# Optimization experiments

Measured on AMD Instinct MI355X. Metric: run time of the kernel, lower is better.

## Reference

```python
import jax, jax.numpy as jnp
import numpy as np

N, L, S, C, H = 4, 2048, 4096, 256, 8
D = C // H          # head dim = 32
HID = 4 * C         # mlp hidden = 1024
LN_EPS = 1e-5
LA_EPS = 1e-6


def _layer_norm(x, g, b):
    m = x.mean(-1, keepdims=True)
    v = ((x - m) ** 2).mean(-1, keepdims=True)
    return (x - m) * jax.lax.rsqrt(v + LN_EPS) * g + b


def _linear_attention(q, k, v):
    # q: [N,L,H,D], k/v: [N,S,H,D]  (elu feature map linear attention)
    Q = jax.nn.elu(q) + 1.0
    K = jax.nn.elu(k) + 1.0
    v_len = v.shape[1]
    KV = jnp.einsum('nshd,nshv->nhdv', K, v / v_len)
    Z = 1.0 / (jnp.einsum('nlhd,nhd->nlh', Q, K.sum(axis=1)) + LA_EPS)
    return jnp.einsum('nlhd,nhdv,nlh->nlhv', Q, KV, Z) * v_len


def setup_inputs() -> dict:
    key = jax.random.key(0)
    ks = jax.random.split(key, 32)
    f32 = jnp.float32
    w = lambda k, *s: (jax.random.normal(k, s, dtype=f32) * 0.02)
    inp = {
        'tgt': jax.random.normal(ks[0], (N, L, C), dtype=f32),
        'memory': jax.random.normal(ks[1], (N, S, C), dtype=f32),
        'tgt_pos': jax.random.normal(ks[2], (N, L, C), dtype=f32),
        'pos_embed': w(ks[3], 1, S, C),
        # layer norms
        'ln1_g': jnp.ones((C,), f32), 'ln1_b': jnp.zeros((C,), f32),
        'ln2_g': jnp.ones((C,), f32), 'ln2_b': jnp.zeros((C,), f32),
        'ln3_g': jnp.ones((C,), f32), 'ln3_b': jnp.zeros((C,), f32),
        # self-attn projections (stored (in,out))
        'wq': w(ks[4], C, C), 'bq': jnp.zeros((C,), f32),
        'wk': w(ks[5], C, C), 'bk': jnp.zeros((C,), f32),
        'wv': w(ks[6], C, C), 'bv': jnp.zeros((C,), f32),
        'w_merge': w(ks[7], C, C),
        # cross-attn (CCAttention) projections
        'cwq': w(ks[8], C, C), 'cbq': jnp.zeros((C,), f32),
        'cwk': w(ks[9], C, C), 'cbk': jnp.zeros((C,), f32),
        'cwv': w(ks[10], C, C), 'cbv': jnp.zeros((C,), f32),
        'cwo': w(ks[11], C, C), 'cbo': jnp.zeros((C,), f32),
        # mlp (fc1 -> dwconv3x3 -> gelu -> fc2)
        'mw1': w(ks[12], C, HID), 'mb1': jnp.zeros((HID,), f32),
        'dw_k': w(ks[13], HID, 1, 3, 3), 'dw_b': jnp.zeros((HID,), f32),
        'mw2': w(ks[14], HID, C), 'mb2': jnp.zeros((C,), f32),
        'num_points': L,
    }
    return inp


def reference(tgt, memory, tgt_pos, pos_embed,
              ln1_g, ln1_b, ln2_g, ln2_b, ln3_g, ln3_b,
              wq, bq, wk, bk, wv, bv, w_merge,
              cwq, cbq, cwk, cbk, cwv, cbv, cwo, cbo,
              mw1, mb1, dw_k, dw_b, mw2, mb2, num_points):
    n, l, c = tgt.shape
    # ---- self attention (linear attention) ----
    tgt2 = _layer_norm(tgt, ln1_g, ln1_b)
    qk = tgt2 + tgt_pos
    q = (qk @ wq + bq).reshape(n, l, H, D)
    k = (qk @ wk + bk).reshape(n, l, H, D)
    v = (tgt2 @ wv + bv).reshape(n, l, H, D)
    msg = _linear_attention(q, k, v).reshape(n, l, c) @ w_merge
    tgt = tgt + msg  # dropout is identity in eval
    # ---- cross attention (CCAttention, softmax MHA) ----
    tgt2 = _layer_norm(tgt, ln2_g, ln2_b)
    mem = memory + pos_embed
    cq = (tgt2 @ cwq + cbq).reshape(n, l, H, D)
    ck = (mem @ cwk + cbk).reshape(n, -1, H, D)
    cv = (mem @ cwv + cbv).reshape(n, -1, H, D)
    scale = D ** -0.5
    attn = jax.nn.softmax(jnp.einsum('nlhd,nshd->nhls', cq, ck) * scale, axis=-1)
    cmsg = jnp.einsum('nhls,nshd->nlhd', attn, cv).reshape(n, l, c) @ cwo + cbo
    tgt = tgt + cmsg
    # ---- MLP with depthwise conv over (num_points, 1) grid ----
    x = _layer_norm(tgt, ln3_g, ln3_b)
    h = x @ mw1 + mb1                                   # [n,l,HID]
    hi = h.transpose(0, 2, 1).reshape(n, HID, num_points, 1)
    hi = jax.lax.conv_general_dilated(
        hi, dw_k, window_strides=(1, 1), padding=((1, 1), (1, 1)),
        feature_group_count=HID,
        dimension_numbers=('NCHW', 'OIHW', 'NCHW'))
    hi = hi + dw_b[None, :, None, None]
    h = hi.reshape(n, HID, l).transpose(0, 2, 1)
    h = jax.nn.gelu(h, approximate=False)
    mlp_out = h @ mw2 + mb2
    return tgt + mlp_out
```

## Files before the change

kernel.cpp:

```cpp
#include <hip/hip_runtime.h>
#include <hip/hip_bf16.h>
#include <math.h>

#define NB 4
#define LL 2048
#define SS 4096
#define CC 256
#define HH 8
#define DD 32
#define HIDN 1024
#define NSPLIT 2

using bf16 = __hip_bfloat16;
typedef __attribute__((ext_vector_type(8))) short short8;
typedef __attribute__((ext_vector_type(4))) short short4v;
typedef __attribute__((ext_vector_type(4))) float floatx4;

__device__ __forceinline__ float b2f(bf16 x) { return __bfloat162float(x); }
__device__ __forceinline__ short f2bs(float x) {
    bf16 h = __float2bfloat16(x);
    return *(short*)&h;
}
__device__ __forceinline__ short f2bs_fast(float x) {
    return (short)(__float_as_uint(x) >> 16);
}
__device__ __forceinline__ float s2f(short s) {
    bf16 h = *(bf16*)&s;
    return __bfloat162float(h);
}

#if __has_builtin(__builtin_amdgcn_exp2f)
#define EXP2(x) __builtin_amdgcn_exp2f(x)
#else
#define EXP2(x) exp2f(x)
#endif

__device__ __forceinline__ bool probe_f32(const unsigned* p) {
    return p[0] == 0x3F800000u;
}
__device__ __forceinline__ float ldx(const void* p, size_t i, bool f32m) {
    return f32m ? ((const float*)p)[i] : b2f(((const bf16*)p)[i]);
}

__global__ __launch_bounds__(256)
void zero_kernel(float* __restrict__ p, int n) {
    int i = blockIdx.x * 256 + threadIdx.x;
    if (i < n) p[i] = 0.0f;
}

struct WPack { const void* p[10]; };

__global__ __launch_bounds__(256)
void wprep_kernel(WPack pk, short* __restrict__ dst,
                  const unsigned* __restrict__ probe) {
    const bool f32m = probe_f32(probe);
    const int z = blockIdx.z;
    const int K = (z == 9) ? 1024 : 256;
    const int N = (z == 8) ? 1024 : 256;
    const size_t off = (z < 8) ? (size_t)z * 65536 : (z == 8 ? 524288u : 786432u);
    const int k0 = blockIdx.y * 64, n0 = blockIdx.x * 64;
    if (k0 >= K || n0 >= N) return;
    __shared__ float T[64][65];
    const void* src = pk.p[z];
    const int tid = threadIdx.x;
    #pragma unroll
    for (int p = 0; p < 16; ++p) {
        int idx = tid + p * 256;
        int r = idx >> 6, c = idx & 63;
        T[r][c] = ldx(src, (size_t)(k0 + r) * N + n0 + c, f32m);
    }
    __syncthreads();
    short* d = dst + off;
    #pragma unroll
    for (int p = 0; p < 16; ++p) {
        int idx = tid + p * 256;
        int c2 = idx >> 6, r2 = idx & 63;
        d[(size_t)(n0 + c2) * K + k0 + r2] = f2bs(T[r2][c2]);
    }
}

__global__ __launch_bounds__(256)
void ln_kernel(const void* __restrict__ xr, const float* __restrict__ xf,
               const void* __restrict__ g, const void* __restrict__ bta,
               const void* __restrict__ pos,
               short* __restrict__ y, short* __restrict__ y2,
               const unsigned* __restrict__ probe) {
    const bool f32m = probe_f32(probe);
    const int row = blockIdx.x;
    const int c = threadIdx.x;
    const size_t base = (size_t)row * CC;
    float x = xr ? ldx(xr, base + c, f32m) : xf[base + c];
    float a = x, b = x * x;
    #pragma unroll
    for (int off = 32; off; off >>= 1) {
        a += __shfl_down(a, off);
        b += __shfl_down(b, off);
    }
    __shared__ float sa[4], sb[4];
    if ((c & 63) == 0) { sa[c >> 6] = a; sb[c >> 6] = b; }
    __syncthreads();
    float s1 = sa[0] + sa[1] + sa[2] + sa[3];
    float s2 = sb[0] + sb[1] + sb[2] + sb[3];
    float mean = s1 * (1.0f / CC);
    float var = s2 * (1.0f / CC) - mean * mean;
    float inv = rsqrtf(var + 1e-5f);
    float yv = (x - mean) * inv * ldx(g, c, f32m) + ldx(bta, c, f32m);
    y[base + c] = f2bs(yv);
    if (y2) y2[base + c] = f2bs(yv + ldx(pos, base + c, f32m));
}

__global__ __launch_bounds__(256)
void addpos_kernel(const void* __restrict__ mem, const void* __restrict__ pos,
                   short* __restrict__ out, const unsigned* __restrict__ probe) {
    const bool f32m = probe_f32(probe);
    const int row = blockIdx.x;
    const int c = threadIdx.x;
    const int s = row & (SS - 1);
    out[(size_t)row * CC + c] =
        f2bs(ldx(mem, (size_t)row * CC + c, f32m) + ldx(pos, (size_t)s * CC + c, f32m));
}

template <int BM, int BN, int EPI, int OUTMODE, int TRANSC2>
__global__ __launch_bounds__(256)
void gemm_mfma_kernel(const short* __restrict__ A, const short* __restrict__ Bt,
                      const void* __restrict__ bias, const void* __restrict__ bias2,
                      const float* __restrict__ residF, const void* __restrict__ residR,
                      void* __restrict__ Cout, void* __restrict__ Cout2,
                      int M, int N, int K, const unsigned* __restrict__ probe) {
    const bool f32m = probe_f32(probe);
    constexpr int WM = BM / 2, AI = WM / 16;
    constexpr int WN = BN / 2, BJ = WN / 16;
    constexpr int ACH = (BM == 128) ? 4 : 2;
    constexpr int BCH = (BN == 128) ? 4 : 2;
    __shared__ __attribute__((aligned(16))) short As[BM][72];
    __shared__ __attribute__((aligned(16))) short Bs[BN][72];
    const int tid = threadIdx.x;
    const int ln = tid & 15, quad = (tid >> 4) & 3, w = tid >> 6;
    const int wm = (w & 1) * WM, wn = (w >> 1) * WN;
    const int bm = blockIdx.y * BM, bn = blockIdx.x * BN;
    const int ar = (BM == 128) ? (tid >> 1) : (tid >> 2);
    const int ac = (BM == 128) ? ((tid & 1) * 32) : ((tid & 3) * 16);
    const int br = (BN == 128) ? (tid >> 1) : (tid >> 2);
    const int bc = (BN == 128) ? ((tid & 1) * 32) : ((tid & 3) * 16);

    short8 pa[ACH], pb[BCH];
    {
        const short* ag = &A[(size_t)(bm + ar) * K + ac];
        #pragma unroll
        for (int t = 0; t < ACH; ++t) pa[t] = *(const short8*)(ag + t * 8);
        const short* bg = &Bt[(size_t)(bn + br) * K + bc];
        #pragma unroll
        for (int t = 0; t < BCH; ++t) pb[t] = *(const short8*)(bg + t * 8);
    }
    floatx4 acc[AI][BJ] = {};
    for (int k0 = 0; k0 < K; k0 += 64) {
        #pragma unroll
        for (int t = 0; t < ACH; ++t) *(short8*)&As[ar][ac + t * 8] = pa[t];
        #pragma unroll
        for (int t = 0; t < BCH; ++t) *(short8*)&Bs[br][bc + t * 8] = pb[t];
        if (k0 + 64 < K) {
            const short* ag = &A[(size_t)(bm + ar) * K + k0 + 64 + ac];
            #pragma unroll
            for (int t = 0; t < ACH; ++t) pa[t] = *(const short8*)(ag + t * 8);
            const short* bg = &Bt[(size_t)(bn + br) * K + k0 + 64 + bc];
            #pragma unroll
            for (int t = 0; t < BCH; ++t) pb[t] = *(const short8*)(bg + t * 8);
        }
        __syncthreads();
        #pragma unroll
        for (int ks = 0; ks < 2; ++ks) {
            short8 af[AI], bf[BJ];
            #pragma unroll
            for (int i = 0; i < AI; ++i)
                af[i] = *(const short8*)&As[wm + i * 16 + ln][ks * 32 + quad * 8];
            #pragma unroll
            for (int j = 0; j < BJ; ++j)
                bf[j] = *(const short8*)&Bs[wn + j * 16 + ln][ks * 32 + quad * 8];
            #pragma unroll
            for (int i = 0; i < AI; ++i)
                #pragma unroll
                for (int j = 0; j < BJ; ++j)
                    acc[i][j] = __builtin_amdgcn_mfma_f32_16x16x32_bf16(af[i], bf[j], acc[i][j], 0, 0, 0);
        }
        __syncthreads();
    }
    #pragma unroll
    for (int i = 0; i < AI; ++i)
        #pragma unroll
        for (int j = 0; j < BJ; ++j) {
            const int gr0 = bm + wm + i * 16 + quad * 4;
            const int gc = bn + wn + j * 16 + ln;
            const bool hi = (Cout2 != nullptr) && (gc >= 256);
            const int col = hi ? gc - 256 : gc;
            const int sN = Cout2 ? 256 : N;
            void* co = hi ? Cout2 : Cout;
            const void* bb = hi ? bias2 : bias;
            float vv[4];
            #pragma unroll
            for (int r = 0; r < 4; ++r) {
                float v = acc[i][j][r];
                if (bb) v += ldx(bb, col, f32m);
                if (EPI == 1) v = (v > 0.0f) ? (v + 1.0f) : __expf(v);
                const size_t o = (size_t)(gr0 + r) * sN + col;
                if (residF) v += residF[o];
                if (residR) v += ldx(residR, o, f32m);
                vv[r] = v;
            }
            if (TRANSC2 && hi) {
                const int nb = gr0 >> 12;
                const int s = gr0 & (SS - 1);
                short4v pk4 = {f2bs(vv[0]), f2bs(vv[1]), f2bs(vv[2]), f2bs(vv[3])};
                *(short4v*)&((short*)co)[((size_t)nb * CC + col) * SS + s] = pk4;
            } else {
                #pragma unroll
                for (int r = 0; r < 4; ++r) {
                    const size_t o = (size_t)(gr0 + r) * sN + col;
                    if (OUTMODE == 0) ((float*)co)[o] = vv[r];
                    else if (OUTMODE == 2) ((short*)co)[o] = f2bs(vv[r]);
                    else {
                        if (f32m) ((float*)co)[o] = vv[r];
                        else      ((bf16*)co)[o] = __float2bfloat16(vv[r]);
                    }
                }
            }
        }
}

#define KVSPLIT 16
__global__ __launch_bounds__(256)
void linattn_kv_kernel(const float* __restrict__ Kp, const float* __restrict__ Vp,
                       float* __restrict__ KV, float* __restrict__ Ksum) {
    const int h = blockIdx.x, n = blockIdx.y, z = blockIdx.z;
    __shared__ __attribute__((aligned(16))) float Kt[64][33];
    __shared__ __attribute__((aligned(16))) float Vt[64][32];
    const int tid = threadIdx.x;
    const int d = tid >> 3, e0 = (tid & 7) * 4;
    const int sbeg = z * (LL / KVSPLIT), send = sbeg + (LL / KVSPLIT);
    float acc[4] = {}, ks = 0.0f;
    for (int s0 = sbeg; s0 < send; s0 += 64) {
        #pragma unroll
        for (int p = 0; p < 8; ++p) {
            int idx = tid + p * 256;
            int r = idx >> 5, c = idx & 31;
            size_t gaddr = (size_t)((n * LL) + s0 + r) * CC + h * DD + c;
            Kt[r][c] = Kp[gaddr];
            Vt[r][c] = Vp[gaddr];
        }
        __syncthreads();
        for (int s = 0; s < 64; ++s) {
            float kd = Kt[s][d];
            ks += kd;
            float4 v4 = *(const float4*)&Vt[s][e0];
            acc[0] += kd * v4.x; acc[1] += kd * v4.y;
            acc[2] += kd * v4.z; acc[3] += kd * v4.w;
        }
        __syncthreads();
    }
    float* kvp = &KV[(size_t)((n * HH + h) * DD + d) * DD + e0];
    atomicAdd(&kvp[0], acc[0]); atomicAdd(&kvp[1], acc[1]);
    atomicAdd(&kvp[2], acc[2]); atomicAdd(&kvp[3], acc[3]);
    if ((tid & 7) == 0) atomicAdd(&Ksum[(n * HH + h) * DD + d], ks);
}

__global__ __launch_bounds__(256)
void linattn_out_kernel(const float* __restrict__ Qp, const float* __restrict__ KV,
                        const float* __restrict__ Ksum, short* __restrict__ Out) {
    const int lt = blockIdx.x, h = blockIdx.y, n = blockIdx.z;
    __shared__ float KVs[32][33];
    __shared__ float Ks[32];
    __shared__ float Qs[64][33];
    const int tid = threadIdx.x;
    for (int p = 0; p < 4; ++p) {
        int idx = tid + p * 256;
        KVs[idx >> 5][idx & 31] = KV[(size_t)(n * HH + h) * (DD * DD) + idx];
    }
    if (tid < 32) Ks[tid] = Ksum[(n * HH + h) * DD + tid];
    for (int p = 0; p < 8; ++p) {
        int idx = tid + p * 256;
        int r = idx >> 5, c = idx & 31;
        Qs[r][c] = Qp[(size_t)((n * LL) + lt * 64 + r) * CC + h * DD + c];
    }
    __syncthreads();
    const int e = tid & 31;
    for (int ii = 0; ii < 8; ++ii) {
        const int i = (tid >> 5) + ii * 8;
        float num = 0.0f, den = 0.0f;
        for (int d = 0; d < 32; ++d) {
            float q = Qs[i][d];
            num += q * KVs[d][e];
            den += q * Ks[d];
        }
        Out[(size_t)((n * LL) + lt * 64 + i) * CC + h * DD + e] = f2bs(num / (den + 1e-6f));
    }
}

__global__ __launch_bounds__(256)
void flash_mfma_kernel(const short* __restrict__ Q, const short* __restrict__ K,
                       const short* __restrict__ V,
                       float* __restrict__ Of, float* __restrict__ Lp) {
    const int lt = blockIdx.x, h = blockIdx.y;
    const int n = blockIdx.z >> 1, sp = blockIdx.z & 1;
    const int tid = threadIdx.x;
    const int ln = tid & 15;
    const int quad = (tid >> 4) & 3;
    const int w = tid >> 6;
    const int NT = NB * LL;
    const float qscale = 0.17677669529663687f * 1.4426950408889634f;

    __shared__ __attribute__((aligned(16))) short Qs[64][40];
    __shared__ __attribute__((aligned(16))) short Ks[64][40];
    __shared__ __attribute__((aligned(16))) short Vp[32][72];

    {
        const int r = tid >> 2, c0 = (tid & 3) * 8;
        short8 qv = *(const short8*)&Q[(size_t)((n * LL) + lt * 64 + r) * CC + h * DD + c0];
        short tmp[8];
        #pragma unroll
        for (int j = 0; j < 8; ++j) tmp[j] = f2bs(s2f(qv[j]) * qscale);
        *(short8*)&Qs[r][c0] = *(short8*)tmp;
    }
    __syncthreads();

    short8 bQ = *(const short8*)&Qs[w * 16 + ln][quad * 8];

    float l_sum = 0.0f;
    floatx4 o0 = {0.f, 0.f, 0.f, 0.f};
    floatx4 o1 = {0.f, 0.f, 0.f, 0.f};
    const floatx4 zinit = {-24.f, -24.f, -24.f, -24.f};

    const int r_st = tid >> 2, c0_st = (tid & 3) * 8;
    const int e_st = tid >> 3, m_st = tid & 7;
    const int K32 = (m_st >> 2) * 32;
    const int h4 = ((m_st >> 1) & 1) * 4;
    const int q0s = (2 * m_st) & 3;
    const int slotA = K32 + q0s * 8 + h4;
    const int slotB = K32 + (q0s + 1) * 8 + h4;

    const int sbeg = sp * (SS / NSPLIT), send = sbeg + (SS / NSPLIT);
    for (int s0 = sbeg; s0 < send; s0 += 64) {
        *(short8*)&Ks[r_st][c0_st] =
            *(const short8*)&K[(size_t)((n * SS) + s0 + r_st) * CC + h * DD + c0_st];
        {
            short8 vv = *(const short8*)&V[((size_t)n * CC + h * DD + e_st) * SS + s0 + m_st * 8];
            short4v lo = {vv[0], vv[1], vv[2], vv[3]};
            short4v hi = {vv[4], vv[5], vv[6], vv[7]};
            *(short4v*)&Vp[e_st][slotA] = lo;
            *(short4v*)&Vp[e_st][slotB] = hi;
        }
        __syncthreads();

        floatx4 sc[4];
        #pragma unroll
        for (int g = 0; g < 4; ++g) {
            short8 aK = *(const short8*)&Ks[g * 16 + ln][quad * 8];
            sc[g] = __builtin_amdgcn_mfma_f32_16x16x32_bf16(aK, bQ, zinit, 0, 0, 0);
        }

        #pragma unroll
        for (int ks = 0; ks < 2; ++ks) {
            short tmp[8];
            #pragma unroll
            for (int j = 0; j < 8; ++j) {
                float p = EXP2(sc[2 * ks + (j >> 2)][j & 3]);
                l_sum += p;
                tmp[j] = f2bs_fast(p);
            }
            short8 aP = *(short8*)tmp;
            short8 bV0 = *(const short8*)&Vp[ln][ks * 32 + quad * 8];
            short8 bV1 = *(const short8*)&Vp[16 + ln][ks * 32 + quad * 8];
            o0 = __builtin_amdgcn_mfma_f32_16x16x32_bf16(aP, bV0, o0, 0, 0, 0);
            o1 = __builtin_amdgcn_mfma_f32_16x16x32_bf16(aP, bV1, o1, 0, 0, 0);
        }
        __syncthreads();
    }

    float s = l_sum;
    s += __shfl_xor(s, 16);
    s += __shfl_xor(s, 32);
    const int rowbase = lt * 64 + w * 16;
    if (quad == 0)
        Lp[((size_t)sp * NT + (size_t)n * LL + rowbase + ln) * HH + h] = s;
    #pragma unroll
    for (int r = 0; r < 4; ++r) {
        const size_t row = (size_t)n * LL + rowbase + quad * 4 + r;
        float* o = &Of[((size_t)sp * NT + row) * CC + h * DD];
        o[ln] = o0[r];
        o[16 + ln] = o1[r];
    }
}

__global__ __launch_bounds__(256)
void flash_merge_kernel(const float* __restrict__ Of, const float* __restrict__ Lp,
                        short* __restrict__ O) {
    const int row = blockIdx.x, c = threadIdx.x, h = c >> 5;
    const size_t NT = (size_t)NB * LL;
    float l = Lp[(size_t)row * HH + h] + Lp[(NT + row) * HH + h];
    float v = Of[(size_t)row * CC + c] + Of[NT * CC + (size_t)row * CC + c];
    O[(size_t)row * CC + c] = f2bs(v / l);
}

__global__ __launch_bounds__(256)
void dwconv_gelu_kernel(const short* __restrict__ H1, const void* __restrict__ wk,
                        const void* __restrict__ wb, short* __restrict__ H2,
                        const unsigned* __restrict__ probe) {
    const bool f32m = probe_f32(probe);
    const int row = blockIdx.x;
    const int l = row & (LL - 1);
    const int c0 = threadIdx.x * 4;
    const short* cur = &H1[(size_t)row * HIDN + c0];
    short4v xc = *(const short4v*)cur;
    short4v xm = {}, xp = {};
    if (l > 0)      xm = *(const short4v*)(cur - HIDN);
    if (l < LL - 1) xp = *(const short4v*)(cur + HIDN);
    short r[4];
    #pragma unroll
    for (int j = 0; j < 4; ++j) {
        int ch = c0 + j;
        float wm = ldx(wk, ch * 9 + 1, f32m);
        float w0 = ldx(wk, ch * 9 + 4, f32m);
        float wp = ldx(wk, ch * 9 + 7, f32m);
        float v = s2f(xm[j]) * wm + s2f(xc[j]) * w0 + s2f(xp[j]) * wp + ldx(wb, ch, f32m);
        r[j] = f2bs(0.5f * v * (1.0f + erff(v * 0.70710678118654752f)));
    }
    short4v out = {r[0], r[1], r[2], r[3]};
    *(short4v*)&H2[(size_t)row * HIDN + c0] = out;
}

extern "C" void kernel_launch(void* const* d_in, const int* in_sizes, int n_in,
                              void* d_out, int out_size, void* d_ws, size_t ws_size,
                              hipStream_t stream) {
    const void* tgt      = d_in[0];
    const void* memory   = d_in[1];
    const void* tgt_pos  = d_in[2];
    const void* pos_emb  = d_in[3];
    const void* ln1_g = d_in[4],  *ln1_b = d_in[5];
    const void* ln2_g = d_in[6],  *ln2_b = d_in[7];
    const void* ln3_g = d_in[8],  *ln3_b = d_in[9];
    const void* wq = d_in[10], *bq = d_in[11];
    const void* wk = d_in[12], *bk = d_in[13];
    const void* wv = d_in[14], *bv = d_in[15];
    const void* w_merge = d_in[16];
    const void* cwq = d_in[17], *cbq = d_in[18];
    const void* cwk = d_in[19], *cbk = d_in[20];
    const void* cwv = d_in[21], *cbv = d_in[22];
    const void* cwo = d_in[23], *cbo = d_in[24];
    const void* mw1 = d_in[25], *mb1 = d_in[26];
    const void* dw_k = d_in[27], *dw_b = d_in[28];
    const void* mw2 = d_in[29], *mb2 = d_in[30];
    const unsigned* probe = (const unsigned*)d_in[4];

    char* w = (char*)d_ws;
    const size_t MB = 1024 * 1024;
    short* lnout_b = (short*)(w + 0 * MB);
    short* qk_b    = (short*)(w + 4 * MB);
    float* Tbuf    = (float*)(w + 8 * MB);
    float* phiq    = (float*)(w + 16 * MB);
    float* phik    = (float*)(w + 24 * MB);
    float* vbuf    = (float*)(w + 32 * MB);
    float* KVb     = (float*)(w + 40 * MB);
    float* Ksb     = (float*)(w + 40 * MB + 131072);
    short* cqbuf   = (short*)(w + 41 * MB);
    short* membuf  = (short*)(w + 45 * MB);
    short* ckbuf   = (short*)(w + 53 * MB);
    short* cvT     = (short*)(w + 69 * MB);
    short* flashO  = (short*)(w + 77 * MB);
    short* wT      = (short*)(w + 81 * MB);
    float* Ofb     = (float*)(w + 16 * MB);
    float* Lpb     = (float*)(w + 32 * MB);
    short* H1      = (short*)(w + 16 * MB);
    short* H2      = (short*)(w + 32 * MB);

    short* wqT  = wT + 0 * 65536;
    short* wvT  = wT + 2 * 65536;
    short* wmT  = wT + 3 * 65536;
    short* cwqT = wT + 4 * 65536;
    short* cwkT = wT + 5 * 65536;
    short* cwoT = wT + 7 * 65536;
    short* mw1T = wT + 524288;
    short* mw2T = wT + 786432;

    const int NT = NB * LL;
    const int NS = NB * SS;
    const dim3 blk(256);

    WPack pk;
    pk.p[0] = wq;  pk.p[1] = wk;  pk.p[2] = wv;  pk.p[3] = w_merge;
    pk.p[4] = cwq; pk.p[5] = cwk; pk.p[6] = cwv; pk.p[7] = cwo;
    pk.p[8] = mw1; pk.p[9] = mw2;
    wprep_kernel<<<dim3(16, 16, 10), blk, 0, stream>>>(pk, wT, probe);
    zero_kernel<<<dim3(137), blk, 0, stream>>>(KVb, 35072);

    ln_kernel<<<NT, blk, 0, stream>>>(tgt, nullptr, ln1_g, ln1_b, tgt_pos, lnout_b, qk_b, probe);
    gemm_mfma_kernel<64, 64, 1, 0, 0><<<dim3(8, NT / 64), blk, 0, stream>>>(
        qk_b, wqT, bq, bk, nullptr, nullptr, phiq, phik, NT, 512, CC, probe);
    gemm_mfma_kernel<64, 64, 0, 0, 0><<<dim3(4, NT / 64), blk, 0, stream>>>(
        lnout_b, wvT, bv, nullptr, nullptr, nullptr, vbuf, nullptr, NT, CC, CC, probe);
    linattn_kv_kernel<<<dim3(HH, NB, KVSPLIT), blk, 0, stream>>>(phik, vbuf, KVb, Ksb);
    linattn_out_kernel<<<dim3(LL / 64, HH, NB), blk, 0, stream>>>(phiq, KVb, Ksb, (short*)vbuf);
    gemm_mfma_kernel<64, 64, 0, 0, 0><<<dim3(4, NT / 64), blk, 0, stream>>>(
        (short*)vbuf, wmT, nullptr, nullptr, nullptr, tgt, Tbuf, nullptr, NT, CC, CC, probe);

    ln_kernel<<<NT, blk, 0, stream>>>(nullptr, Tbuf, ln2_g, ln2_b, nullptr, lnout_b, nullptr, probe);
    addpos_kernel<<<NS, blk, 0, stream>>>(memory, pos_emb, membuf, probe);
    gemm_mfma_kernel<64, 64, 0, 2, 0><<<dim3(4, NT / 64), blk, 0, stream>>>(
        lnout_b, cwqT, cbq, nullptr, nullptr, nullptr, cqbuf, nullptr, NT, CC, CC, probe);
    gemm_mfma_kernel<64, 64, 0, 2, 1><<<dim3(8, NS / 64), blk, 0, stream>>>(
        membuf, cwkT, cbk, cbv, nullptr, nullptr, ckbuf, cvT, NS, 512, CC, probe);
    flash_mfma_kernel<<<dim3(LL / 64, HH, NB * NSPLIT), blk, 0, stream>>>(
        cqbuf, ckbuf, cvT, Ofb, Lpb);
    flash_merge_kernel<<<NT, blk, 0, stream>>>(Ofb, Lpb, flashO);
    gemm_mfma_kernel<64, 64, 0, 0, 0><<<dim3(4, NT / 64), blk, 0, stream>>>(
        flashO, cwoT, cbo, nullptr, Tbuf, nullptr, Tbuf, nullptr, NT, CC, CC, probe);

    ln_kernel<<<NT, blk, 0, stream>>>(nullptr, Tbuf, ln3_g, ln3_b, nullptr, lnout_b, nullptr, probe);
    gemm_mfma_kernel<64, 64, 0, 2, 0><<<dim3(16, NT / 64), blk, 0, stream>>>(
        lnout_b, mw1T, mb1, nullptr, nullptr, nullptr, H1, nullptr, NT, HIDN, CC, probe);
    dwconv_gelu_kernel<<<NT, blk, 0, stream>>>(H1, dw_k, dw_b, H2, probe);
    gemm_mfma_kernel<64, 64, 0, 1, 0><<<dim3(4, NT / 64), blk, 0, stream>>>(
        H2, mw2T, mb2, nullptr, Tbuf, nullptr, d_out, nullptr, NT, CC, HIDN, probe);

    (void)in_sizes; (void)n_in; (void)out_size; (void)ws_size;
}
```

Before: 430.8 us.

## Split KV tile across waves in flash kernel and reduce partials in LDS

The cross-attention flash kernel now loads 128 keys per iteration and gives each wave its own 16-key slice of each 64-key half. Each wave keeps all 64 query rows (four Q fragments in registers) instead of one 16-row slice. This halves the number of loop iterations and barriers per tile and amortizes loads over more MFMA work. The cost is more accumulator registers per thread and a serialized cross-wave reduction of partial outputs and row sums through shared memory, with a barrier per wave, at the end.

```diff
diff --git a/kernel.cpp b/kernel.cpp
--- a/kernel.cpp
+++ b/kernel.cpp
@@ -308,8 +308,8 @@
     const float qscale = 0.17677669529663687f * 1.4426950408889634f;
 
     __shared__ __attribute__((aligned(16))) short Qs[64][40];
-    __shared__ __attribute__((aligned(16))) short Ks[64][40];
-    __shared__ __attribute__((aligned(16))) short Vp[32][72];
+    __shared__ __attribute__((aligned(16))) short Ks[128][40];
+    __shared__ __attribute__((aligned(16))) short Vp[4][32][36];
 
     {
         const int r = tid >> 2, c0 = (tid & 3) * 8;
@@ -321,71 +321,106 @@
     }
     __syncthreads();
 
-    short8 bQ = *(const short8*)&Qs[w * 16 + ln][quad * 8];
-
-    float l_sum = 0.0f;
-    floatx4 o0 = {0.f, 0.f, 0.f, 0.f};
-    floatx4 o1 = {0.f, 0.f, 0.f, 0.f};
+    short8 bQ[4];
+    #pragma unroll
+    for (int f = 0; f < 4; ++f)
+        bQ[f] = *(const short8*)&Qs[f * 16 + ln][quad * 8];
+
+    float l_sum[4] = {0.f, 0.f, 0.f, 0.f};
+    floatx4 oacc[4][2] = {};
     const floatx4 zinit = {-24.f, -24.f, -24.f, -24.f};
 
-    const int r_st = tid >> 2, c0_st = (tid & 3) * 8;
+    const int kr = tid >> 1, kc = (tid & 1) * 16;
     const int e_st = tid >> 3, m_st = tid & 7;
-    const int K32 = (m_st >> 2) * 32;
-    const int h4 = ((m_st >> 1) & 1) * 4;
-    const int q0s = (2 * m_st) & 3;
-    const int slotA = K32 + q0s * 8 + h4;
-    const int slotB = K32 + (q0s + 1) * 8 + h4;
+    const int wv_st = m_st & 3, tt4 = (m_st >> 2) * 4;
 
     const int sbeg = sp * (SS / NSPLIT), send = sbeg + (SS / NSPLIT);
-    for (int s0 = sbeg; s0 < send; s0 += 64) {
-        *(short8*)&Ks[r_st][c0_st] =
-            *(const short8*)&K[(size_t)((n * SS) + s0 + r_st) * CC + h * DD + c0_st];
+    for (int s0 = sbeg; s0 < send; s0 += 128) {
         {
-            short8 vv = *(const short8*)&V[((size_t)n * CC + h * DD + e_st) * SS + s0 + m_st * 8];
-            short4v lo = {vv[0], vv[1], vv[2], vv[3]};
-            short4v hi = {vv[4], vv[5], vv[6], vv[7]};
-            *(short4v*)&Vp[e_st][slotA] = lo;
-            *(short4v*)&Vp[e_st][slotB] = hi;
-        }
-        __syncthreads();
-
-        floatx4 sc[4];
-        #pragma unroll
-        for (int g = 0; g < 4; ++g) {
-            short8 aK = *(const short8*)&Ks[g * 16 + ln][quad * 8];
-            sc[g] = __builtin_amdgcn_mfma_f32_16x16x32_bf16(aK, bQ, zinit, 0, 0, 0);
-        }
-
-        #pragma unroll
-        for (int ks = 0; ks < 2; ++ks) {
+            const short* kg = &K[(size_t)((n * SS) + s0 + kr) * CC + h * DD + kc];
+            *(short8*)&Ks[kr][kc]     = *(const short8*)kg;
+            *(short8*)&Ks[kr][kc + 8] = *(const short8*)(kg + 8);
+        }
+        {
+            const short* vg = &V[((size_t)n * CC + h * DD + e_st) * SS + s0 + m_st * 16];
+            short8 v0 = *(const short8*)vg;
+            short8 v1 = *(const short8*)(vg + 8);
+            short* dst = &Vp[wv_st][e_st][0];
+            *(short4v*)&dst[tt4]      = (short4v){v0[0], v0[1], v0[2], v0[3]};
+            *(short4v*)&dst[8 + tt4]  = (short4v){v0[4], v0[5], v0[6], v0[7]};
+            *(short4v*)&dst[16 + tt4] = (short4v){v1[0], v1[1], v1[2], v1[3]};
+            *(short4v*)&dst[24 + tt4] = (short4v){v1[4], v1[5], v1[6], v1[7]};
+        }
+        __syncthreads();
+
+        floatx4 sc[2][4];
+        #pragma unroll
+        for (int t = 0; t < 2; ++t) {
+            short8 aK = *(const short8*)&Ks[t * 64 + w * 16 + ln][quad * 8];
+            #pragma unroll
+            for (int f = 0; f < 4; ++f)
+                sc[t][f] = __builtin_amdgcn_mfma_f32_16x16x32_bf16(aK, bQ[f], zinit, 0, 0, 0);
+        }
+
+        short8 bV0 = *(const short8*)&Vp[w][ln][quad * 8];
+        short8 bV1 = *(const short8*)&Vp[w][16 + ln][quad * 8];
+        #pragma unroll
+        for (int f = 0; f < 4; ++f) {
             short tmp[8];
             #pragma unroll
             for (int j = 0; j < 8; ++j) {
-                float p = EXP2(sc[2 * ks + (j >> 2)][j & 3]);
-                l_sum += p;
+                float p = EXP2(sc[j >> 2][f][j & 3]);
+                l_sum[f] += p;
                 tmp[j] = f2bs_fast(p);
             }
             short8 aP = *(short8*)tmp;
-            short8 bV0 = *(const short8*)&Vp[ln][ks * 32 + quad * 8];
-            short8 bV1 = *(const short8*)&Vp[16 + ln][ks * 32 + quad * 8];
-            o0 = __builtin_amdgcn_mfma_f32_16x16x32_bf16(aP, bV0, o0, 0, 0, 0);
-            o1 = __builtin_amdgcn_mfma_f32_16x16x32_bf16(aP, bV1, o1, 0, 0, 0);
-        }
-        __syncthreads();
-    }
-
-    float s = l_sum;
-    s += __shfl_xor(s, 16);
-    s += __shfl_xor(s, 32);
-    const int rowbase = lt * 64 + w * 16;
-    if (quad == 0)
-        Lp[((size_t)sp * NT + (size_t)n * LL + rowbase + ln) * HH + h] = s;
-    #pragma unroll
-    for (int r = 0; r < 4; ++r) {
-        const size_t row = (size_t)n * LL + rowbase + quad * 4 + r;
-        float* o = &Of[((size_t)sp * NT + row) * CC + h * DD];
-        o[ln] = o0[r];
-        o[16 + ln] = o1[r];
+            oacc[f][0] = __builtin_amdgcn_mfma_f32_16x16x32_bf16(aP, bV0, oacc[f][0], 0, 0, 0);
+            oacc[f][1] = __builtin_amdgcn_mfma_f32_16x16x32_bf16(aP, bV1, oacc[f][1], 0, 0, 0);
+        }
+        __syncthreads();
+    }
+
+    float lw[4];
+    #pragma unroll
+    for (int f = 0; f < 4; ++f) {
+        float s = l_sum[f];
+        s += __shfl_xor(s, 16);
+        s += __shfl_xor(s, 32);
+        lw[f] = s;
+    }
+    __syncthreads();
+    float (*Ored)[33] = (float(*)[33])&Ks[0][0];
+    float* Lred = (float*)&Vp[0][0][0];
+    for (int ww = 0; ww < 4; ++ww) {
+        if (w == ww) {
+            #pragma unroll
+            for (int f = 0; f < 4; ++f) {
+                #pragma unroll
+                for (int r = 0; r < 4; ++r) {
+                    const int row = f * 16 + quad * 4 + r;
+                    if (ww == 0) {
+                        Ored[row][ln] = oacc[f][0][r];
+                        Ored[row][16 + ln] = oacc[f][1][r];
+                    } else {
+                        Ored[row][ln] += oacc[f][0][r];
+                        Ored[row][16 + ln] += oacc[f][1][r];
+                    }
+                }
+                if (quad == 0) {
+                    const int l = f * 16 + ln;
+                    if (ww == 0) Lred[l] = lw[f]; else Lred[l] += lw[f];
+                }
+            }
+        }
+        __syncthreads();
+    }
+    {
+        const int row = tid >> 2, c0 = (tid & 3) * 8;
+        float* o = &Of[((size_t)sp * NT + (size_t)n * LL + lt * 64 + row) * CC + h * DD + c0];
+        #pragma unroll
+        for (int j = 0; j < 8; ++j) o[j] = Ored[row][c0 + j];
+        if (tid < 64)
+            Lp[((size_t)sp * NT + (size_t)n * LL + lt * 64 + tid) * HH + h] = Lred[tid];
     }
 }
 
```

Measured after the change: 447.7 us. +3.9%, slower.
